# Kernel tuning notes

Measured on AMD Instinct MI355X. Metric: run time of the kernel, lower is better.

The kernel has to match this reference:

```python
import jax, jax.numpy as jnp
import numpy as np

R, C, B, E, H = 128, 256, 1, 768, 12
DK = E // H


def setup_inputs() -> dict:
    key = jax.random.key(0)
    ks = jax.random.split(key, 6)
    x = jax.random.normal(ks[0], (R, C, B, E), dtype=jnp.float32)
    padding_mask = jnp.zeros((B, R, C), dtype=bool)  # all positions valid
    w_scale = 0.02
    Wq = jax.random.normal(ks[1], (E, E), dtype=jnp.float32) * w_scale
    Wk = jax.random.normal(ks[2], (E, E), dtype=jnp.float32) * w_scale
    Wv = jax.random.normal(ks[3], (E, E), dtype=jnp.float32) * w_scale
    Wo = jax.random.normal(ks[4], (E, E), dtype=jnp.float32) * w_scale
    bq = jnp.zeros((E,), jnp.float32)
    bk = jnp.zeros((E,), jnp.float32)
    bv = jnp.zeros((E,), jnp.float32)
    bo = jnp.zeros((E,), jnp.float32)
    return {"x": x, "padding_mask": padding_mask, "Wq": Wq, "bq": bq,
            "Wk": Wk, "bk": bk, "Wv": Wv, "bv": bv, "Wo": Wo, "bo": bo}


def reference(x, padding_mask, Wq, bq, Wk, bk, Wv, bv, Wo, bo):
    # x: (n_rows=i, n_cols=c, batch=n, embed)
    n_rows, n_cols, batch, embed = x.shape
    d_k = embed // H
    scaling = d_k ** -0.5
    # torch Linear: y = x @ W.T + b
    q = (x @ Wq.T + bq).reshape(n_rows, n_cols, batch, H, d_k) * scaling
    k = (x @ Wk.T + bk).reshape(n_rows, n_cols, batch, H, d_k)
    v = (x @ Wv.T + bv).reshape(n_rows, n_cols, batch, H, d_k)
    # attention over the row axis, independent per column and batch
    attn = jnp.einsum('icnhd,jcnhd->hcnij', q, k)  # (H, C, B, R, R)
    # padding_mask (n, i, c) -> (1, c, n, 1, j), masked keys get -10000
    m = jnp.transpose(padding_mask, (2, 0, 1))[None, :, :, None, :]
    attn = jnp.where(m, jnp.float32(-10000.0), attn)
    probs = jax.nn.softmax(attn, axis=-1)
    # dropout is identity in eval/reference mode
    ctx = jnp.einsum('hcnij,jcnhd->icnhd', probs, v)
    ctx = ctx.reshape(n_rows, n_cols, batch, embed)
    out = ctx @ Wo.T + bo
    return out, probs
```

## Files before the change

### kernel.cpp

```cpp
#include <hip/hip_runtime.h>
#include <hip/hip_bf16.h>

typedef __attribute__((ext_vector_type(8))) short bf16x8;
typedef __attribute__((ext_vector_type(4))) float f32x4;
typedef __attribute__((ext_vector_type(8))) unsigned short u16x8;

#define RR 128
#define CC 256
#define EE 768
#define HH 12
#define DKK 64
#define NQKV 2304

__device__ __forceinline__ unsigned short f2bf(float f) {
  union { float f; unsigned u; } v; v.f = f;
  unsigned u = v.u;
  unsigned r = (u + 0x7fffu + ((u >> 16) & 1u)) >> 16;
  return (unsigned short)r;
}

__device__ __forceinline__ void gload16(const unsigned short* g, char* l) {
  __builtin_amdgcn_global_load_lds((const __attribute__((address_space(1))) void*)g,
                                   (__attribute__((address_space(3))) void*)l, 16, 0, 0);
}

__global__ void cast_all(const float* __restrict__ x, const float* __restrict__ w0,
                         const float* __restrict__ w1, const float* __restrict__ w2,
                         const float* __restrict__ w3, unsigned short* __restrict__ xb,
                         unsigned short* __restrict__ wdst) {
  int b = blockIdx.x;
  const float* src;
  unsigned short* dst;
  int t;
  if (b < 12288) {
    src = x; dst = xb; t = b * 256 + (int)threadIdx.x;
  } else {
    int bb = b - 12288;
    int m = bb / 288;
    src = (m == 0) ? w0 : (m == 1) ? w1 : (m == 2) ? w2 : w3;
    dst = wdst + (size_t)m * 589824;
    t = (bb - m * 288) * 256 + (int)threadIdx.x;
  }
  const float4* s = (const float4*)src + (size_t)t * 2;
  float4 a = s[0], bq = s[1];
  u16x8 o;
  o[0] = f2bf(a.x); o[1] = f2bf(a.y); o[2] = f2bf(a.z); o[3] = f2bf(a.w);
  o[4] = f2bf(bq.x); o[5] = f2bf(bq.y); o[6] = f2bf(bq.z); o[7] = f2bf(bq.w);
  *(u16x8*)(dst + (size_t)t * 8) = o;
}


#define SBAR() do { __builtin_amdgcn_sched_barrier(0); __builtin_amdgcn_s_barrier(); } while (0)
#define SBAR2() do { __builtin_amdgcn_sched_barrier(0); __builtin_amdgcn_s_barrier(); __builtin_amdgcn_sched_barrier(0); } while (0)
#define WAITL() do { asm volatile("s_waitcnt lgkmcnt(0)" ::: "memory"); __builtin_amdgcn_sched_barrier(0); } while (0)
#define WAITV(N) asm volatile("s_waitcnt vmcnt(" #N ")" ::: "memory")

template <int OUTMODE>
__global__ __launch_bounds__(512, 2) void gemm256(
    const unsigned short* __restrict__ A, const unsigned short* __restrict__ Bw,
    void* __restrict__ OutP, const float* __restrict__ bias0,
    const float* __restrict__ bias1, const float* __restrict__ bias2) {
  __shared__ __align__(16) char smem[131072];
  const int nwg = gridDim.x;
  const int chunk = nwg >> 3;
  const int swz = ((int)blockIdx.x & 7) * chunk + ((int)blockIdx.x >> 3);
  const int bm = swz % 128, bn = swz / 128;
  const int r0 = bm << 8, c0 = bn << 8;

  const int tid = threadIdx.x;
  const int w = tid >> 6, lane = tid & 63;
  const int wr = w >> 2, wc = w & 3;
  const int lr = lane & 15, lg = lane >> 4;
  const int l8 = lane >> 3, l7 = lane & 7;
  const int swzc = (l7 ^ (l8 & 7)) << 3;
  const unsigned short* pa = A + (size_t)(r0 + l8) * EE + swzc;
  const unsigned short* pb = Bw + (size_t)(c0 + l8) * EE + swzc;
  const int j0 = w, j1 = w + 8;

  const int aoff = (wr << 14) + (lr << 7);
  const int boff = 32768 + ((wc >> 1) << 14) + ((wc & 1) << 13) + (lr << 7);
  const int sw0 = ((0 + lg) ^ (lr & 7)) << 4;
  const int sw1 = ((4 + lg) ^ (lr & 7)) << 4;

  f32x4 acc[8][4] = {};
  bf16x8 aA[4], aB[4], aC[4], aD[4], bA[4], bB[4];

#define STAGE(s, H, t)                                                        \
  do {                                                                        \
    const unsigned short* _src = ((H) < 2 ? pa : pb) +                        \
        (size_t)(((H) & 1) * 128) * EE + (size_t)(t) * 64;                    \
    char* _d = smem + (s) * 65536 + ((H) >= 2 ? 32768 : 0) + ((H) & 1) * 16384; \
    gload16(_src + (size_t)j0 * 8 * EE, _d + j0 * 1024);                      \
    gload16(_src + (size_t)j1 * 8 * EE, _d + j1 * 1024);                      \
  } while (0)

#define RD_A(dst, g, SW, s)                                                   \
  _Pragma("unroll") for (int _m = 0; _m < 4; ++_m)                            \
      dst[_m] = *(const bf16x8*)(smem + (s) * 65536 + aoff + (g) * 8192 +     \
                                 _m * 2048 + (SW));

#define RD_B(dst, SW, s)                                                      \
  _Pragma("unroll") for (int _n = 0; _n < 4; ++_n)                            \
      dst[_n] = *(const bf16x8*)(smem + (s) * 65536 + boff + _n * 2048 + (SW));

#define MM(g, ar, br)                                                         \
  do {                                                                        \
    __builtin_amdgcn_s_setprio(1);                                            \
    _Pragma("unroll") for (int _i = 0; _i < 4; ++_i)                          \
        _Pragma("unroll") for (int _j = 0; _j < 4; ++_j)                      \
            acc[(g) * 4 + _i][_j] = __builtin_amdgcn_mfma_f32_16x16x32_bf16(  \
                ar[_i], br[_j], acc[(g) * 4 + _i][_j], 0, 0, 0);              \
    __builtin_amdgcn_s_setprio(0);                                            \
  } while (0)

#define ITER(ii, LASTF)                                                        \
  do {                                                                         \
    const int t0 = 2 * (ii), t1 = t0 + 1;                                      \
     RD_A(aA, 0, sw0, 0); RD_B(bA, sw0, 0); STAGE(1, 1, t1);             \
    SBAR(); WAITL(); MM(0, aA, bA); SBAR2();                                   \
     RD_A(aB, 1, sw0, 0); RD_A(aC, 0, sw1, 0); STAGE(1, 2, t1);          \
    SBAR(); WAITL(); MM(1, aB, bA); SBAR2();                                   \
     RD_B(bB, sw1, 0); RD_A(aD, 1, sw1, 0); STAGE(1, 3, t1);             \
    SBAR(); WAITL(); MM(0, aC, bB); SBAR2();                                   \
     if (!(LASTF)) { STAGE(0, 0, t0 + 2); WAITV(2); } else { WAITV(0); } \
    SBAR(); WAITL(); MM(1, aD, bB); SBAR2();                                   \
     RD_A(aA, 0, sw0, 1); RD_B(bA, sw0, 1);                              \
    if (!(LASTF)) STAGE(0, 1, t0 + 2);                                         \
    SBAR(); WAITL(); MM(0, aA, bA); SBAR2();                                   \
     RD_A(aB, 1, sw0, 1); RD_A(aC, 0, sw1, 1);                           \
    if (!(LASTF)) STAGE(0, 2, t0 + 2);                                         \
    SBAR(); WAITL(); MM(1, aB, bA); SBAR2();                                   \
     RD_B(bB, sw1, 1); RD_A(aD, 1, sw1, 1);                              \
    if (!(LASTF)) STAGE(0, 3, t0 + 2);                                         \
    SBAR(); WAITL(); MM(0, aC, bB); SBAR2();                                   \
     if (!(LASTF)) { STAGE(1, 0, t1 + 2); WAITV(2); }                    \
    SBAR(); WAITL(); MM(1, aD, bB); SBAR2();                                   \
  } while (0)

  STAGE(0, 0, 0); STAGE(0, 1, 0); STAGE(0, 2, 0); STAGE(0, 3, 0);
  STAGE(1, 0, 1);
  WAITV(2);
  SBAR2();

#pragma unroll 1
  for (int it = 0; it < 5; ++it) { ITER(it, 0); }
  ITER(5, 1);

#undef STAGE
#undef RD_A
#undef RD_B
#undef MM
#undef ITER

  if constexpr (OUTMODE == 1) {
    unsigned short* sm = (unsigned short*)smem;
    const int mat = bn / 3;
    const float scale = (mat == 0) ? 0.125f : 1.0f;
    const float* bp = (mat == 0) ? bias0 : (mat == 1 ? bias1 : bias2);
    const int cb = c0 - mat * 768;
    float bv4[4];
#pragma unroll
    for (int n = 0; n < 4; ++n) bv4[n] = bp[cb + (wc << 6) + (n << 4) + lr];
#pragma unroll
    for (int m = 0; m < 8; ++m)
#pragma unroll
      for (int n = 0; n < 4; ++n)
#pragma unroll
        for (int r = 0; r < 4; ++r) {
          int row = (wr << 7) + (m << 4) + (lg << 2) + r;
          int col = (wc << 6) + (n << 4) + lr;
          sm[row * 256 + col] = f2bf((acc[m][n][r] + bv4[n]) * scale);
        }
    __syncthreads();
    unsigned short* outm = (unsigned short*)OutP + (size_t)mat * 25165824;
    const int hbase = cb >> 6;
    const int i_idx = r0 >> 8;
#pragma unroll
    for (int p = 0; p < 16; ++p) {
      int idx = p * 512 + tid;
      int row = idx >> 5;
      int hl = (idx >> 3) & 3;
      int d8 = idx & 7;
      *(u16x8*)(outm + ((((size_t)(row * HH + hbase + hl)) << 7 | i_idx) << 6) + d8 * 8) =
          *(const u16x8*)(sm + row * 256 + hl * 64 + d8 * 8);
    }
  } else {
    float* out = (float*)OutP;
    float bv4[4];
#pragma unroll
    for (int n = 0; n < 4; ++n) bv4[n] = bias0[c0 + (wc << 6) + (n << 4) + lr];
#pragma unroll
    for (int m = 0; m < 8; ++m)
#pragma unroll
      for (int n = 0; n < 4; ++n)
#pragma unroll
        for (int r = 0; r < 4; ++r) {
          int u = r0 + (wr << 7) + (m << 4) + (lg << 2) + r;
          int t = ((u & 127) << 8) | (u >> 7);
          int col = (wc << 6) + (n << 4) + lr;
          out[(size_t)t * EE + c0 + col] = acc[m][n][r] + bv4[n];
        }
  }
}

__global__ __launch_bounds__(512, 2) void attn_col(
    const unsigned short* __restrict__ qatt, const unsigned short* __restrict__ katt,
    const unsigned short* __restrict__ vatt, const unsigned char* __restrict__ pmask,
    float* __restrict__ probs, unsigned short* __restrict__ ctx) {
  __shared__ unsigned short sm[53248];
  const int c = blockIdx.x;
  const int tid = threadIdx.x;
  const int w = tid >> 6, lane = tid & 63;
  const int lr = lane & 15, lg = lane >> 4;
  const int j0 = tid >> 3;
  const int j1 = 64 + j0;
  const int d00 = (tid & 7) << 3;
  const int kst0 = j0 * 72 + d00, kst1 = j1 * 72 + d00;
  unsigned short* ps = sm + 35840;
  const size_t cb12 = (size_t)c * HH;

  unsigned char pmv[8];
#pragma unroll
  for (int n = 0; n < 8; ++n) pmv[n] = pmask[(size_t)((n << 4) + lr) * CC + c];

  {
    const unsigned short* kb = katt + (cb12 << 13);
    const unsigned short* vb = vatt + (cb12 << 13);
    bf16x8 k0 = *(const bf16x8*)(kb + j0 * 64 + d00);
    bf16x8 k1 = *(const bf16x8*)(kb + j1 * 64 + d00);
    bf16x8 v0 = *(const bf16x8*)(vb + j0 * 64 + d00);
    bf16x8 v1 = *(const bf16x8*)(vb + j1 * 64 + d00);
    *(bf16x8*)(sm + kst0) = k0;
    *(bf16x8*)(sm + kst1) = k1;
    unsigned short* vt0 = sm + 18432;
#pragma unroll
    for (int u = 0; u < 8; ++u) vt0[(d00 + u) * 136 + j0] = (unsigned short)v0[u];
#pragma unroll
    for (int u = 0; u < 8; ++u) vt0[(d00 + u) * 136 + j1] = (unsigned short)v1[u];
  }
  bf16x8 qf0, qf1;
  {
    const unsigned short* qb = qatt + (cb12 << 13);
    qf0 = *(const bf16x8*)(qb + ((w << 4) + lr) * 64 + (lg << 3));
    qf1 = *(const bf16x8*)(qb + ((w << 4) + lr) * 64 + 32 + (lg << 3));
  }
  __syncthreads();

  int cur = 0;
#pragma unroll 1
  for (int h = 0; h < HH; ++h) {
    const unsigned short* ksc = sm + cur * 9216;
    const unsigned short* vtc = sm + 18432 + cur * 8704;

    bf16x8 kr0{}, kr1{}, vr0{}, vr1{}, qn0{}, qn1{};
    const bool pf = (h + 1 < HH);
    if (pf) {
      const unsigned short* kb = katt + ((cb12 + h + 1) << 13);
      const unsigned short* vb = vatt + ((cb12 + h + 1) << 13);
      const unsigned short* qb = qatt + ((cb12 + h + 1) << 13);
      kr0 = *(const bf16x8*)(kb + j0 * 64 + d00);
      kr1 = *(const bf16x8*)(kb + j1 * 64 + d00);
      vr0 = *(const bf16x8*)(vb + j0 * 64 + d00);
      vr1 = *(const bf16x8*)(vb + j1 * 64 + d00);
      qn0 = *(const bf16x8*)(qb + ((w << 4) + lr) * 64 + (lg << 3));
      qn1 = *(const bf16x8*)(qb + ((w << 4) + lr) * 64 + 32 + (lg << 3));
    }

    f32x4 s[8] = {};
#pragma unroll
    for (int kk = 0; kk < 2; ++kk) {
      bf16x8 kf[8];
#pragma unroll
      for (int n = 0; n < 8; ++n)
        kf[n] = *(const bf16x8*)&ksc[((n << 4) + lr) * 72 + kk * 32 + (lg << 3)];
      bf16x8 q = kk ? qf1 : qf0;
#pragma unroll
      for (int n = 0; n < 8; ++n)
        s[n] = __builtin_amdgcn_mfma_f32_16x16x32_bf16(q, kf[n], s[n], 0, 0, 0);
    }

#pragma unroll
    for (int n = 0; n < 8; ++n) {
      if (pmv[n]) {
        f32x4 neg = {-10000.0f, -10000.0f, -10000.0f, -10000.0f};
        s[n] = neg;
      }
    }

    f32x4 mxv = s[0];
#pragma unroll
    for (int n = 1; n < 8; ++n)
#pragma unroll
      for (int r = 0; r < 4; ++r) mxv[r] = fmaxf(mxv[r], s[n][r]);
#pragma unroll
    for (int r = 0; r < 4; ++r) {
      float t = mxv[r];
      t = fmaxf(t, __shfl_xor(t, 1));
      t = fmaxf(t, __shfl_xor(t, 2));
      t = fmaxf(t, __shfl_xor(t, 4));
      t = fmaxf(t, __shfl_xor(t, 8));
      mxv[r] = t;
    }
    f32x4 sum = {};
#pragma unroll
    for (int n = 0; n < 8; ++n)
#pragma unroll
      for (int r = 0; r < 4; ++r) {
        float e = exp2f((s[n][r] - mxv[r]) * 1.44269504f);
        s[n][r] = e;
        sum[r] += e;
      }
    float inv_[4];
#pragma unroll
    for (int r = 0; r < 4; ++r) {
      float t = sum[r];
      t += __shfl_xor(t, 1);
      t += __shfl_xor(t, 2);
      t += __shfl_xor(t, 4);
      t += __shfl_xor(t, 8);
      inv_[r] = __builtin_amdgcn_rcpf(t);
    }

    const size_t pbase = ((size_t)h * CC + c) << 14;
#pragma unroll
    for (int n = 0; n < 8; ++n)
#pragma unroll
      for (int r = 0; r < 4; ++r) {
        float pv = s[n][r] * inv_[r];
        int i = (w << 4) + (lg << 2) + r;
        int j = (n << 4) + lr;
        probs[pbase + (size_t)i * 128 + j] = pv;
        ps[i * 136 + j] = f2bf(pv);
      }

    f32x4 o[4] = {};
#pragma unroll
    for (int kk = 0; kk < 4; ++kk) {
      bf16x8 pa = *(const bf16x8*)&ps[((w << 4) + lr) * 136 + kk * 32 + (lg << 3)];
      bf16x8 vbr[4];
#pragma unroll
      for (int n = 0; n < 4; ++n)
        vbr[n] = *(const bf16x8*)&vtc[((n << 4) + lr) * 136 + kk * 32 + (lg << 3)];
#pragma unroll
      for (int n = 0; n < 4; ++n)
        o[n] = __builtin_amdgcn_mfma_f32_16x16x32_bf16(pa, vbr[n], o[n], 0, 0, 0);
    }

    if (pf) {
      unsigned short* ksn = sm + (cur ^ 1) * 9216;
      unsigned short* vtn = sm + 18432 + (cur ^ 1) * 8704;
      *(bf16x8*)(ksn + kst0) = kr0;
      *(bf16x8*)(ksn + kst1) = kr1;
#pragma unroll
      for (int u = 0; u < 8; ++u) vtn[(d00 + u) * 136 + j0] = (unsigned short)vr0[u];
#pragma unroll
      for (int u = 0; u < 8; ++u) vtn[(d00 + u) * 136 + j1] = (unsigned short)vr1[u];
      qf0 = qn0; qf1 = qn1;
    }

    unsigned short* bandc = ps + ((w << 4) * 136);
#pragma unroll
    for (int n = 0; n < 4; ++n)
#pragma unroll
      for (int r = 0; r < 4; ++r)
        bandc[((lg << 2) + r) * 64 + (n << 4) + lr] = f2bf(o[n][r]);
#pragma unroll
    for (int q = 0; q < 2; ++q) {
      int fl = q * 64 + lane;
      int iL = fl >> 3, d8 = fl & 7;
      *(u16x8*)(ctx + ((size_t)c * 128 + (w << 4) + iL) * EE + h * 64 + d8 * 8) =
          *(const u16x8*)(bandc + iL * 64 + d8 * 8);
    }

    __syncthreads();
    cur ^= 1;
  }
}

extern "C" void kernel_launch(void* const* d_in, const int* in_sizes, int n_in,
                              void* d_out, int out_size, void* d_ws, size_t ws_size,
                              hipStream_t stream) {
  const float* x = (const float*)d_in[0];
  const unsigned char* pm = (const unsigned char*)d_in[1];
  const float* Wq = (const float*)d_in[2];
  const float* bq = (const float*)d_in[3];
  const float* Wk = (const float*)d_in[4];
  const float* bk = (const float*)d_in[5];
  const float* Wv = (const float*)d_in[6];
  const float* bv = (const float*)d_in[7];
  const float* Wo = (const float*)d_in[8];
  const float* bo = (const float*)d_in[9];

  unsigned short* ws = (unsigned short*)d_ws;
  unsigned short* xb = ws;
  unsigned short* qkv = xb + 25165824;
  unsigned short* wcast = qkv + 75497472;

  float* outp = (float*)d_out;
  float* probs = outp + 25165824;

  cast_all<<<13440, 256, 0, stream>>>(x, Wq, Wk, Wv, Wo, xb, wcast);
  gemm256<1><<<1152, 512, 0, stream>>>(xb, wcast, (void*)qkv, bq, bk, bv);
  attn_col<<<CC, 512, 0, stream>>>(qkv, qkv + 25165824, qkv + 50331648,
                                   pm, probs, xb );
  gemm256<0><<<384, 512, 0, stream>>>(xb, wcast + 1769472, (void*)outp, bo,
                                      nullptr, nullptr);
}
```

Before: 326.6 us.

## Load K via direct global-to-LDS copies with XOR swizzle, swizzle V transpose

K tiles are now fetched with global_load_lds straight into shared memory, replacing the register round-trip. The padded layout becomes an unpadded one with an XOR swizzle on 16-byte slots. The transposed V stores and reads also get an XOR swizzle on the key index, to cut LDS bank conflicts on the scattered 2-byte writes. This shrinks shared memory slightly and frees registers, but the async LDS loads need correct waits before the next head reads them.

```diff
diff --git a/kernel.cpp b/kernel.cpp
--- a/kernel.cpp
+++ b/kernel.cpp
@@ -207,16 +207,16 @@
     const unsigned short* __restrict__ qatt, const unsigned short* __restrict__ katt,
     const unsigned short* __restrict__ vatt, const unsigned char* __restrict__ pmask,
     float* __restrict__ probs, unsigned short* __restrict__ ctx) {
-  __shared__ unsigned short sm[53248];
+  __shared__ unsigned short sm[51200];
   const int c = blockIdx.x;
   const int tid = threadIdx.x;
   const int w = tid >> 6, lane = tid & 63;
   const int lr = lane & 15, lg = lane >> 4;
   const int j0 = tid >> 3;
-  const int j1 = 64 + j0;
   const int d00 = (tid & 7) << 3;
-  const int kst0 = j0 * 72 + d00, kst1 = j1 * 72 + d00;
-  unsigned short* ps = sm + 35840;
+  const int kslot = (((tid & 7) ^ ((tid >> 3) & 7)) << 3);
+  const int dblk = (d00 >> 3) & 7;
+  unsigned short* ps = sm + 33792;
   const size_t cb12 = (size_t)c * HH;
 
   unsigned char pmv[8];
@@ -225,18 +225,18 @@
 
   {
     const unsigned short* kb = katt + (cb12 << 13);
+    gload16(kb + j0 * 64 + kslot, (char*)sm + tid * 16);
+    gload16(kb + (64 + j0) * 64 + kslot, (char*)sm + 8192 + tid * 16);
     const unsigned short* vb = vatt + (cb12 << 13);
-    bf16x8 k0 = *(const bf16x8*)(kb + j0 * 64 + d00);
-    bf16x8 k1 = *(const bf16x8*)(kb + j1 * 64 + d00);
     bf16x8 v0 = *(const bf16x8*)(vb + j0 * 64 + d00);
-    bf16x8 v1 = *(const bf16x8*)(vb + j1 * 64 + d00);
-    *(bf16x8*)(sm + kst0) = k0;
-    *(bf16x8*)(sm + kst1) = k1;
-    unsigned short* vt0 = sm + 18432;
-#pragma unroll
-    for (int u = 0; u < 8; ++u) vt0[(d00 + u) * 136 + j0] = (unsigned short)v0[u];
-#pragma unroll
-    for (int u = 0; u < 8; ++u) vt0[(d00 + u) * 136 + j1] = (unsigned short)v1[u];
+    bf16x8 v1 = *(const bf16x8*)(vb + (64 + j0) * 64 + d00);
+    unsigned short* vt0 = sm + 16384;
+    int jx0 = j0 ^ (dblk << 3);
+    int jx1 = (64 + j0) ^ (dblk << 3);
+#pragma unroll
+    for (int u = 0; u < 8; ++u) vt0[(d00 + u) * 136 + jx0] = (unsigned short)v0[u];
+#pragma unroll
+    for (int u = 0; u < 8; ++u) vt0[(d00 + u) * 136 + jx1] = (unsigned short)v1[u];
   }
   bf16x8 qf0, qf1;
   {
@@ -249,34 +249,32 @@
   int cur = 0;
 #pragma unroll 1
   for (int h = 0; h < HH; ++h) {
-    const unsigned short* ksc = sm + cur * 9216;
-    const unsigned short* vtc = sm + 18432 + cur * 8704;
-
-    bf16x8 kr0{}, kr1{}, vr0{}, vr1{}, qn0{}, qn1{};
+    const unsigned short* ksc = sm + cur * 8192;
+    const unsigned short* vtc = sm + 16384 + cur * 8704;
     const bool pf = (h + 1 < HH);
+
+    bf16x8 vr0{}, vr1{}, qn0{}, qn1{};
     if (pf) {
       const unsigned short* kb = katt + ((cb12 + h + 1) << 13);
+      char* ksn = (char*)sm + (cur ^ 1) * 16384;
+      gload16(kb + j0 * 64 + kslot, ksn + tid * 16);
+      gload16(kb + (64 + j0) * 64 + kslot, ksn + 8192 + tid * 16);
       const unsigned short* vb = vatt + ((cb12 + h + 1) << 13);
       const unsigned short* qb = qatt + ((cb12 + h + 1) << 13);
-      kr0 = *(const bf16x8*)(kb + j0 * 64 + d00);
-      kr1 = *(const bf16x8*)(kb + j1 * 64 + d00);
       vr0 = *(const bf16x8*)(vb + j0 * 64 + d00);
-      vr1 = *(const bf16x8*)(vb + j1 * 64 + d00);
+      vr1 = *(const bf16x8*)(vb + (64 + j0) * 64 + d00);
       qn0 = *(const bf16x8*)(qb + ((w << 4) + lr) * 64 + (lg << 3));
       qn1 = *(const bf16x8*)(qb + ((w << 4) + lr) * 64 + 32 + (lg << 3));
     }
 
     f32x4 s[8] = {};
 #pragma unroll
-    for (int kk = 0; kk < 2; ++kk) {
-      bf16x8 kf[8];
-#pragma unroll
-      for (int n = 0; n < 8; ++n)
-        kf[n] = *(const bf16x8*)&ksc[((n << 4) + lr) * 72 + kk * 32 + (lg << 3)];
-      bf16x8 q = kk ? qf1 : qf0;
-#pragma unroll
-      for (int n = 0; n < 8; ++n)
-        s[n] = __builtin_amdgcn_mfma_f32_16x16x32_bf16(q, kf[n], s[n], 0, 0, 0);
+    for (int n = 0; n < 8; ++n) {
+      const unsigned short* krow = ksc + ((n << 4) + lr) * 64;
+      bf16x8 k0 = *(const bf16x8*)(krow + ((lg ^ (lr & 7)) << 3));
+      bf16x8 k1 = *(const bf16x8*)(krow + (((4 + lg) ^ (lr & 7)) << 3));
+      s[n] = __builtin_amdgcn_mfma_f32_16x16x32_bf16(qf0, k0, s[n], 0, 0, 0);
+      s[n] = __builtin_amdgcn_mfma_f32_16x16x32_bf16(qf1, k1, s[n], 0, 0, 0);
     }
 
 #pragma unroll
@@ -339,22 +337,24 @@
       bf16x8 pa = *(const bf16x8*)&ps[((w << 4) + lr) * 136 + kk * 32 + (lg << 3)];
       bf16x8 vbr[4];
 #pragma unroll
-      for (int n = 0; n < 4; ++n)
-        vbr[n] = *(const bf16x8*)&vtc[((n << 4) + lr) * 136 + kk * 32 + (lg << 3)];
+      for (int n = 0; n < 4; ++n) {
+        int d = (n << 4) + lr;
+        int jb = (kk * 32 + (lg << 3)) ^ ((((d >> 3) & 7)) << 3);
+        vbr[n] = *(const bf16x8*)&vtc[d * 136 + jb];
+      }
 #pragma unroll
       for (int n = 0; n < 4; ++n)
         o[n] = __builtin_amdgcn_mfma_f32_16x16x32_bf16(pa, vbr[n], o[n], 0, 0, 0);
     }
 
     if (pf) {
-      unsigned short* ksn = sm + (cur ^ 1) * 9216;
-      unsigned short* vtn = sm + 18432 + (cur ^ 1) * 8704;
-      *(bf16x8*)(ksn + kst0) = kr0;
-      *(bf16x8*)(ksn + kst1) = kr1;
-#pragma unroll
-      for (int u = 0; u < 8; ++u) vtn[(d00 + u) * 136 + j0] = (unsigned short)vr0[u];
-#pragma unroll
-      for (int u = 0; u < 8; ++u) vtn[(d00 + u) * 136 + j1] = (unsigned short)vr1[u];
+      unsigned short* vtn = sm + 16384 + (cur ^ 1) * 8704;
+      int jx0 = j0 ^ (dblk << 3);
+      int jx1 = (64 + j0) ^ (dblk << 3);
+#pragma unroll
+      for (int u = 0; u < 8; ++u) vtn[(d00 + u) * 136 + jx0] = (unsigned short)vr0[u];
+#pragma unroll
+      for (int u = 0; u < 8; ++u) vtn[(d00 + u) * 136 + jx1] = (unsigned short)vr1[u];
       qf0 = qn0; qf1 = qn1;
     }
 
```

Result: no change. 323.9 us (median of 2 runs) (-0.8%).
